# Optimization experiments

Measured on AMD Instinct MI355X. Metric: run time of the kernel, lower is better.

The kernel has to match this reference:

```python
import jax, jax.numpy as jnp
import numpy as np

# ---- config derived from init_kwargs ----
D_MODEL = 768
QK = 64            # qk_dim
HEADDIM = 64
D_INNER = 1536     # round(2.0 * d_model)
H = D_INNER // HEADDIM  # 24 heads
NUM_BC = 2         # share_BC_for_two_graphs -> 4 - 2
NUM_DT = 2         # share_dt_for_two_graphs -> 4 - 2
D_IN_PROJ = 2 * D_INNER + QK * 2 * NUM_BC + H * 2 * NUM_DT  # 3424
CONV_DIM = D_INNER + QK * 2 * NUM_BC                        # 1792
IH, IW = 32, 32
EPS = 1e-5


def setup_inputs() -> dict:
    key = jax.random.key(0)
    ks = jax.random.split(key, 4)
    Bsz, L = 32, IH * IW
    return {
        "u": jax.random.normal(ks[0], (Bsz, L, D_MODEL), jnp.float32),
        "w_in": jax.random.normal(ks[1], (D_IN_PROJ, D_MODEL), jnp.float32) * 0.02,
        "conv_w": jax.random.normal(ks[2], (CONV_DIM, 1, 3, 3), jnp.float32) * 0.1,
        "conv_b": jnp.zeros((CONV_DIM,), jnp.float32),
        "norm_w": jnp.ones((D_INNER,), jnp.float32),
        "w_out": jax.random.normal(ks[3], (D_MODEL, D_INNER), jnp.float32) * 0.02,
    }


def _ssm_scan(dt, Bm, Cm, x):
    """Selective scan. dt:(b,L,H)  Bm,Cm:(b,L,N)  x:(b,L,H,P) -> y:(b,L,H,P)"""
    a = jnp.exp(-dt)  # per-step decay (A = -1 per head)

    def step(h, inp):
        a_t, dt_t, B_t, C_t, x_t = inp
        h = a_t[:, :, None, None] * h + jnp.einsum('bh,bn,bhp->bhnp', dt_t, B_t, x_t)
        y = jnp.einsum('bn,bhnp->bhp', C_t, h)
        return h, y

    b, _, nh = dt.shape
    N, P = Bm.shape[-1], x.shape[-1]
    h0 = jnp.zeros((b, nh, N, P), dt.dtype)
    mv = lambda t: jnp.moveaxis(t, 1, 0)  # put L in scan position
    _, ys = jax.lax.scan(step, h0, (mv(a), mv(dt), mv(Bm), mv(Cm), mv(x)))
    return jnp.moveaxis(ys, 0, 1)


def reference(u, w_in, conv_w, conv_b, norm_w, w_out):
    b, L, _ = u.shape
    zxBCdt = u @ w_in.T  # (b, L, D_IN_PROJ)
    z, xBC, dt = jnp.split(
        zxBCdt, [D_INNER, 2 * D_INNER + QK * 2 * NUM_BC], axis=-1)

    # depthwise 3x3 conv2d over the (IH, IW) token grid, NCHW layout
    x4 = jnp.moveaxis(xBC.reshape(b, IH, IW, CONV_DIM), 3, 1)
    x4 = jax.lax.conv_general_dilated(
        x4, conv_w, window_strides=(1, 1), padding=[(1, 1), (1, 1)],
        feature_group_count=CONV_DIM)
    x4 = jax.nn.silu(x4 + conv_b[None, :, None, None])
    xBC = jnp.moveaxis(x4, 1, 3).reshape(b, L, CONV_DIM)

    x, Bc, Cc = jnp.split(xBC, [D_INNER, D_INNER + NUM_BC * QK], axis=-1)
    xh = x.reshape(b, L, H, HEADDIM)
    Bc = Bc.reshape(b, L, NUM_BC, QK)
    Cc = Cc.reshape(b, L, NUM_BC, QK)
    # dt: 2 graphs x 2 directions, each per-head
    dt_all = jax.nn.softplus(dt.reshape(b, L, 2 * NUM_DT, H))

    y = jnp.zeros((b, L, H, HEADDIM), u.dtype)
    for k in range(2 * NUM_DT):       # fixed small loop: graph x direction
        g, rev = k // 2, k % 2
        dtk, Bk, Ck, xk = dt_all[:, :, k], Bc[:, :, g], Cc[:, :, g], xh
        if rev:  # backward direction over the token sequence
            dtk, Bk, Ck, xk = (jnp.flip(t, 1) for t in (dtk, Bk, Ck, xk))
        yk = _ssm_scan(dtk, Bk, Ck, xk)
        y = y + (jnp.flip(yk, 1) if rev else yk)

    y = y.reshape(b, L, D_INNER)
    # gated RMSNorm (Mamba2-style): norm(y * silu(z)) * weight
    yg = y * jax.nn.silu(z)
    yn = yg * jax.lax.rsqrt(jnp.mean(yg * yg, axis=-1, keepdims=True) + EPS)
    yn = yn * norm_w
    return yn @ w_out.T  # (b, L, d_model)
```

## Files before the change

kernel.cpp:

```cpp
#include <hip/hip_runtime.h>
#include <hip/hip_bf16.h>
#include <stdint.h>


#define D_MODEL 768
#define D_INNER 1536
#define NH 24
#define D_IN_PROJ 3424
#define CONV_DIM 1792
#define NDT 96
#define LSEQ 1024

typedef __bf16 bf16x8 __attribute__((ext_vector_type(8)));
typedef float f32x4 __attribute__((ext_vector_type(4)));

__global__ void cvt_kernel(const float* __restrict__ src, __hip_bfloat16* __restrict__ dst, int n4) {
    int i = blockIdx.x * 256 + threadIdx.x;
    if (i < n4) {
        float4 v = ((const float4*)src)[i];
        __hip_bfloat162 lo, hi;
        lo.x = __float2bfloat16(v.x); lo.y = __float2bfloat16(v.y);
        hi.x = __float2bfloat16(v.z); hi.y = __float2bfloat16(v.w);
        ((__hip_bfloat162*)dst)[2*i]   = lo;
        ((__hip_bfloat162*)dst)[2*i+1] = hi;
    }
}

__global__ void repack_w(const float* __restrict__ cw, float* __restrict__ wT) {
    int i = blockIdx.x * 256 + threadIdx.x;
    if (i < CONV_DIM * 9) {
        int c = i / 9, t = i % 9;
        wT[t * CONV_DIM + c] = cw[i];
    }
}

__device__ __forceinline__ void gl_lds16(const __hip_bfloat16* g, __hip_bfloat16* l) {
    __builtin_amdgcn_global_load_lds(
        (const __attribute__((address_space(1))) void*)g,
        (__attribute__((address_space(3))) void*)l, 16, 0, 0);
}

template<int MODE>
__global__ __launch_bounds__(256) void gemm_bt(
    const __hip_bfloat16* __restrict__ A,
    const __hip_bfloat16* __restrict__ Bt,
    float* __restrict__ OutF,
    __hip_bfloat16* __restrict__ Z, __hip_bfloat16* __restrict__ XBC, float* __restrict__ DT,
    int M, int N, int K)
{
    __shared__ __hip_bfloat16 As[128*32];
    __shared__ __hip_bfloat16 Bs[128*32];
    const int tid  = threadIdx.x;
    const int wave = tid >> 6, lane = tid & 63;
    const int bm = blockIdx.x * 128, bn = blockIdx.y * 128;
    const int wm = (wave >> 1) * 64, wn = (wave & 1) * 64;
    f32x4 acc[4][4] = {};
    const int lrow = lane >> 2;
    const int lcol = (lane & 3) * 8;
    const int fr = lane & 15, fk = (lane >> 4) * 8;
    const int ktiles = K >> 5;
    for (int kt = 0; kt < ktiles; ++kt) {
        const int kofs = kt * 32;
        #pragma unroll
        for (int cc = 0; cc < 2; ++cc) {
            int r = (wave*2 + cc)*16 + lrow;
            gl_lds16(A + (size_t)(bm + r)*K + kofs + lcol, &As[r*32 + lcol]);
            int gn = bn + r; if (gn > N-1) gn = N-1;
            gl_lds16(Bt + (size_t)gn*K + kofs + lcol, &Bs[r*32 + lcol]);
        }
        __syncthreads();
        bf16x8 af[4], bfr[4];
        #pragma unroll
        for (int i = 0; i < 4; ++i)
            af[i] = *reinterpret_cast<const bf16x8*>(&As[(wm + i*16 + fr)*32 + fk]);
        #pragma unroll
        for (int j = 0; j < 4; ++j)
            bfr[j] = *reinterpret_cast<const bf16x8*>(&Bs[(wn + j*16 + fr)*32 + fk]);
        #pragma unroll
        for (int i = 0; i < 4; ++i)
            #pragma unroll
            for (int j = 0; j < 4; ++j)
                acc[i][j] = __builtin_amdgcn_mfma_f32_16x16x32_bf16(af[i], bfr[j], acc[i][j], 0, 0, 0);
        __syncthreads();
    }
    const int er = (lane >> 4) * 4;
    const int ec = lane & 15;
    #pragma unroll
    for (int i = 0; i < 4; ++i) {
        #pragma unroll
        for (int j = 0; j < 4; ++j) {
            #pragma unroll
            for (int r = 0; r < 4; ++r) {
                int row = bm + wm + i*16 + er + r;
                int col = bn + wn + j*16 + ec;
                if (col < N) {
                    float v = acc[i][j][r];
                    if (MODE == 0) {
                        OutF[(size_t)row*N + col] = v;
                    } else {
                        if (col < D_INNER)
                            Z[(size_t)row*D_INNER + col] = __float2bfloat16(v);
                        else if (col < 3328)
                            XBC[(size_t)row*CONV_DIM + (col - D_INNER)] = __float2bfloat16(v);
                        else
                            DT[(size_t)row*NDT + (col - 3328)] = v;
                    }
                }
            }
        }
    }
}

__global__ __launch_bounds__(256) void conv_kernel(
    const __hip_bfloat16* __restrict__ xbc,
    const float* __restrict__ wT,
    const float* __restrict__ cb,
    __hip_bfloat16* __restrict__ out)
{
    size_t idx = (size_t)blockIdx.x * 256 + threadIdx.x;
    const int cg = (int)(idx % (CONV_DIM / 8));
    const int c = cg * 8;
    size_t bp = idx / (CONV_DIM / 8);
    const int pix = (int)(bp % LSEQ);
    const int b = (int)(bp / LSEQ);
    const int y = pix >> 5, x = pix & 31;
    float acc[8];
    {
        float4 c0 = *(const float4*)(cb + c);
        float4 c1 = *(const float4*)(cb + c + 4);
        acc[0]=c0.x; acc[1]=c0.y; acc[2]=c0.z; acc[3]=c0.w;
        acc[4]=c1.x; acc[5]=c1.y; acc[6]=c1.z; acc[7]=c1.w;
    }
    const size_t rowbase = (size_t)b * LSEQ;
    #pragma unroll
    for (int dy = -1; dy <= 1; ++dy) {
        int yy = y + dy; if (yy < 0 || yy > 31) continue;
        #pragma unroll
        for (int dx = -1; dx <= 1; ++dx) {
            int xx = x + dx; if (xx < 0 || xx > 31) continue;
            const int t = (dy+1)*3 + (dx+1);
            bf16x8 v = *(const bf16x8*)(xbc + (rowbase + yy*32 + xx)*(size_t)CONV_DIM + c);
            float4 w0 = *(const float4*)(wT + t*CONV_DIM + c);
            float4 w1 = *(const float4*)(wT + t*CONV_DIM + c + 4);
            acc[0] += w0.x * (float)v[0];
            acc[1] += w0.y * (float)v[1];
            acc[2] += w0.z * (float)v[2];
            acc[3] += w0.w * (float)v[3];
            acc[4] += w1.x * (float)v[4];
            acc[5] += w1.y * (float)v[5];
            acc[6] += w1.z * (float)v[6];
            acc[7] += w1.w * (float)v[7];
        }
    }
    bf16x8 o;
    #pragma unroll
    for (int i = 0; i < 8; ++i) {
        float s = acc[i] / (1.f + __expf(-acc[i]));
        o[i] = (__bf16)s;
    }
    *(bf16x8*)(out + (rowbase + pix)*(size_t)CONV_DIM + c) = o;
}

#define PADW 72
__device__ __forceinline__ f32x4 mfma16(bf16x8 a, bf16x8 b, f32x4 c) {
    return __builtin_amdgcn_mfma_f32_16x16x32_bf16(a, b, c, 0, 0, 0);
}
__device__ __forceinline__ void bar_lds() {
    asm volatile("s_waitcnt lgkmcnt(0)" ::: "memory");
    __builtin_amdgcn_s_barrier();
    __builtin_amdgcn_sched_barrier(0);
}

__global__ __launch_bounds__(256, 3) void scan_ssd(
    const __bf16* __restrict__ conv,
    const float* __restrict__ dtraw,
    __bf16* __restrict__ yf,
    __bf16* __restrict__ yr)
{
    const int tid = threadIdx.x;
    const int w = tid >> 6, lane = tid & 63;
    const int b = blockIdx.x, h = blockIdx.y, dir = blockIdx.z;
    __bf16* yout = dir ? yr : yf;
    const size_t base = (size_t)b * LSEQ;
    const size_t Rtot = (size_t)gridDim.x * LSEQ;

    __shared__ __align__(16) __bf16 XT[64*PADW];
    __shared__ __align__(16) __bf16 Gs[64*PADW];
    __shared__ __align__(16) __bf16 Ts[64*PADW];
    __shared__ __align__(16) __bf16 HT[64*PADW];
    __shared__ __align__(16) __bf16 Bss[64*64];
    __shared__ float Warr[2][64], Earr[2][64], Wmarr[2][64], Rmarr[2][64];

    f32x4 Hst0[4] = {}, Hst1[4] = {};

    const int srow = tid >> 2;
    const int scol = (tid & 3) * 16;
    const int fr = lane & 15, fkq = (lane >> 4) * 8;
    const int er = (lane >> 4) * 4, ec = lane & 15;
    const int rn = w*16 + fr;
    const int sl = dir ? 63 - srow : srow;

    const int rA0 = dir ? (LSEQ - 64) : 0;
    const ptrdiff_t dRow = (ptrdiff_t)(dir ? -64 : 64) * CONV_DIM;
    const ptrdiff_t dDt  = (ptrdiff_t)(dir ? -64 : 64) * NDT;
    const __bf16* pRow = conv + (base + rA0 + srow) * (size_t)CONV_DIM;
    const __bf16* pC   = conv + (base + rA0 + (dir ? 63 - rn : rn)) * (size_t)CONV_DIM + 1664;
    const float*  pDt  = dtraw + (base + rA0 + (dir ? 63 - lane : lane)) * NDT
                         + (2*(tid >> 6) + dir)*24 + h;
    const int xoff = h*64 + scol;

    bf16x8 pfx0 = *(const bf16x8*)(pRow + xoff);
    bf16x8 pfx1 = *(const bf16x8*)(pRow + xoff + 8);
    bf16x8 pfbA0 = *(const bf16x8*)(pRow + 1536 + scol);
    bf16x8 pfbA1 = *(const bf16x8*)(pRow + 1536 + scol + 8);
    bf16x8 pfbB0 = *(const bf16x8*)(pRow + 1600 + scol);
    bf16x8 pfbB1 = *(const bf16x8*)(pRow + 1600 + scol + 8);
    bf16x8 pfc00 = *(const bf16x8*)(pC + fkq);
    bf16x8 pfc01 = *(const bf16x8*)(pC + 32 + fkq);
    bf16x8 pfc10 = *(const bf16x8*)(pC + 64 + fkq);
    bf16x8 pfc11 = *(const bf16x8*)(pC + 96 + fkq);
    float pfd = 0.f;
    if (tid < 128) pfd = *pDt;

    #pragma unroll 1
    for (int c = 0; c < 16; ++c) {
        const int rA = dir ? (LSEQ - (c+1)*64) : c*64;

        bf16x8 bA0 = pfbA0, bA1 = pfbA1, bB0 = pfbB0, bB1 = pfbB1;
        bf16x8 c00 = pfc00, c01 = pfc01, c10 = pfc10, c11 = pfc11;

        {
            const int tau = sl;
            #pragma unroll
            for (int i = 0; i < 8; ++i) {
                const int p = scol + i;
                XT[p*PADW + (tau ^ (((p >> 3) & 7) << 3))] = pfx0[i];
            }
            #pragma unroll
            for (int i = 0; i < 8; ++i) {
                const int p = scol + 8 + i;
                XT[p*PADW + (tau ^ (((p >> 3) & 7) << 3))] = pfx1[i];
            }
            if (tid < 128) {
                const int g = tid >> 6;
                const int t2 = lane;
                float e = __expf(pfd);
                float dts = __logf(1.f + e);
                float s = dts;
                #pragma unroll
                for (int off = 1; off < 64; off <<= 1) {
                    float v = __shfl_up(s, off, 64);
                    if (lane >= off) s += v;
                }
                float stot = __shfl(s, 63, 64);
                float smid = __shfl(s, 31, 64);
                Warr[g][t2]  = __expf(s - stot) * dts;
                Earr[g][t2]  = __expf(-s);
                Wmarr[g][t2] = __expf(s - smid) * dts;
                Rmarr[g][t2] = __expf(smid - s);
            }
        }
        if (c != 15) {
            pRow += dRow; pC += dRow; pDt += dDt;
            pfx0 = *(const bf16x8*)(pRow + xoff);
            pfx1 = *(const bf16x8*)(pRow + xoff + 8);
            pfbA0 = *(const bf16x8*)(pRow + 1536 + scol);
            pfbA1 = *(const bf16x8*)(pRow + 1536 + scol + 8);
            pfbB0 = *(const bf16x8*)(pRow + 1600 + scol);
            pfbB1 = *(const bf16x8*)(pRow + 1600 + scol + 8);
            pfc00 = *(const bf16x8*)(pC + fkq);
            pfc01 = *(const bf16x8*)(pC + 32 + fkq);
            pfc10 = *(const bf16x8*)(pC + 64 + fkq);
            pfc11 = *(const bf16x8*)(pC + 96 + fkq);
            if (tid < 128) pfd = *pDt;
        }
        bar_lds();

        f32x4 Yacc[4] = {};

        auto group = [&](const int g, f32x4 (&Hst)[4],
                         bf16x8 bR0, bf16x8 bR1, bf16x8 cf0, bf16x8 cf1) {
            {
                const float ws = Warr[g][sl];
                const int rsw = (sl & 7) << 3;
                #pragma unroll
                for (int i = 0; i < 8; ++i) {
                    const int n = scol + i;
                    Ts[n*PADW + (sl ^ (((n >> 3) & 7) << 3))] = (__bf16)((float)bR0[i] * ws);
                }
                #pragma unroll
                for (int i = 0; i < 8; ++i) {
                    const int n = scol + 8 + i;
                    Ts[n*PADW + (sl ^ (((n >> 3) & 7) << 3))] = (__bf16)((float)bR1[i] * ws);
                }
                *(bf16x8*)&Bss[sl*64 + (scol ^ rsw)] = bR0;
                *(bf16x8*)&Bss[sl*64 + ((scol + 8) ^ rsw)] = bR1;
            }
            #pragma unroll
            for (int t4 = 0; t4 < 4; ++t4) {
                const int p = t4*16 + ec;
                #pragma unroll
                for (int j = 0; j < 2; ++j) {
                    const int n = w*16 + er + 2*j;
                    __hip_bfloat162 pr;
                    pr.x = __float2bfloat16(Hst[t4][2*j]);
                    pr.y = __float2bfloat16(Hst[t4][2*j+1]);
                    *(__hip_bfloat162*)&HT[p*PADW + n] = pr;
                }
            }
            bar_lds();
            f32x4 Gacc[4] = {};
            __builtin_amdgcn_s_setprio(1);
            #pragma unroll
            for (int s4 = 0; s4 < 4; ++s4) {
                const int s = s4*16 + fr;
                const int ssw = (s & 7) << 3;
                bf16x8 bb0 = *(const bf16x8*)&Bss[s*64 + (fkq ^ ssw)];
                bf16x8 bb1 = *(const bf16x8*)&Bss[s*64 + ((32 + fkq) ^ ssw)];
                Gacc[s4] = mfma16(cf0, bb0, Gacc[s4]);
                Gacc[s4] = mfma16(cf1, bb1, Gacc[s4]);
            }
            __builtin_amdgcn_s_setprio(0);
            const float e63 = Earr[g][63];
            #pragma unroll
            for (int t4 = 0; t4 < 4; ++t4)
                #pragma unroll
                for (int rr = 0; rr < 4; ++rr) Hst[t4][rr] *= e63;
            float rmv[4];
            #pragma unroll
            for (int rr = 0; rr < 4; ++rr) rmv[rr] = Rmarr[g][w*16 + er + rr];
            #pragma unroll
            for (int s4 = 0; s4 < 4; ++s4) {
                const int s = s4*16 + ec;
                const float wm = Wmarr[g][s];
                #pragma unroll
                for (int rr = 0; rr < 4; ++rr) {
                    const int tau = w*16 + er + rr;
                    float m = (tau >= s) ? wm * rmv[rr] : 0.f;
                    Gs[tau*PADW + s] = (__bf16)(Gacc[s4][rr] * m);
                }
            }
            bf16x8 ga0 = *(const bf16x8*)&Gs[rn*PADW + fkq];
            bf16x8 ga1 = *(const bf16x8*)&Gs[rn*PADW + 32 + fkq];
            const float esc = Earr[g][rn];
            bf16x8 ca0, ca1;
            #pragma unroll
            for (int i = 0; i < 8; ++i) {
                ca0[i] = (__bf16)((float)cf0[i] * esc);
                ca1[i] = (__bf16)((float)cf1[i] * esc);
            }
            const int Sn = ((rn >> 3) & 7) << 3;
            bf16x8 ta0 = *(const bf16x8*)&Ts[rn*PADW + (fkq ^ Sn)];
            bf16x8 ta1 = *(const bf16x8*)&Ts[rn*PADW + ((32 + fkq) ^ Sn)];
            __builtin_amdgcn_s_setprio(1);
            #pragma unroll
            for (int p4 = 0; p4 < 4; ++p4) {
                const int p = p4*16 + fr;
                const int Sp = ((p >> 3) & 7) << 3;
                bf16x8 x0 = *(const bf16x8*)&XT[p*PADW + (fkq ^ Sp)];
                bf16x8 x1 = *(const bf16x8*)&XT[p*PADW + ((32 + fkq) ^ Sp)];
                bf16x8 h0 = *(const bf16x8*)&HT[p*PADW + fkq];
                bf16x8 h1 = *(const bf16x8*)&HT[p*PADW + 32 + fkq];
                Yacc[p4] = mfma16(ga0, x0, Yacc[p4]);
                Yacc[p4] = mfma16(ga1, x1, Yacc[p4]);
                Yacc[p4] = mfma16(ca0, h0, Yacc[p4]);
                Yacc[p4] = mfma16(ca1, h1, Yacc[p4]);
                Hst[p4] = mfma16(ta0, x0, Hst[p4]);
                Hst[p4] = mfma16(ta1, x1, Hst[p4]);
            }
            __builtin_amdgcn_s_setprio(0);
        };

        group(0, Hst0, bA0, bA1, c00, c01);
        bar_lds();
        group(1, Hst1, bB0, bB1, c10, c11);

        #pragma unroll
        for (int p4 = 0; p4 < 4; ++p4)
            #pragma unroll
            for (int rr = 0; rr < 4; ++rr) {
                const int tau = w*16 + er + rr;
                Gs[tau*PADW + p4*16 + ec] = (__bf16)Yacc[p4][rr];
            }
        bar_lds();
        {
            const int rowp = rA + (dir ? 63 - srow : srow);
            bf16x8 y0 = *(const bf16x8*)&Gs[srow*PADW + scol];
            bf16x8 y1 = *(const bf16x8*)&Gs[srow*PADW + scol + 8];
            __bf16* dst = yout + ((size_t)h * Rtot + (base + rowp)) * 64 + scol;
            *(bf16x8*)dst = y0;
            *(bf16x8*)(dst + 8) = y1;
        }
    }
}

__global__ __launch_bounds__(256) void gate_kernel(
    const __hip_bfloat16* __restrict__ yf, const __hip_bfloat16* __restrict__ yr,
    const __hip_bfloat16* __restrict__ z, const float* __restrict__ norm_w,
    __hip_bfloat16* __restrict__ yn)
{
    const int row = blockIdx.x, tid = threadIdx.x;
    const size_t R = gridDim.x;
    const size_t ybase = (size_t)row * D_INNER;
    float yg[6]; float ss = 0.f;
    #pragma unroll
    for (int k = 0; k < 6; ++k) {
        int j = tid + k*256;
        size_t yidx = ((size_t)(j >> 6) * R + row) * 64 + (j & 63);
        float yv = __bfloat162float(yf[yidx]) + __bfloat162float(yr[yidx]);
        float zz = __bfloat162float(z[ybase+j]);
        float g  = yv * (zz / (1.f + __expf(-zz)));
        yg[k] = g; ss += g*g;
    }
    #pragma unroll
    for (int off = 32; off > 0; off >>= 1) ss += __shfl_down(ss, off, 64);
    __shared__ float red[4];
    if ((tid & 63) == 0) red[tid >> 6] = ss;
    __syncthreads();
    float total = red[0] + red[1] + red[2] + red[3];
    float rn = rsqrtf(total * (1.f/1536.f) + 1e-5f);
    #pragma unroll
    for (int k = 0; k < 6; ++k) {
        int j = tid + k*256;
        yn[ybase+j] = __float2bfloat16(yg[k] * rn * norm_w[j]);
    }
}

extern "C" void kernel_launch(void* const* d_in, const int* in_sizes, int n_in,
                              void* d_out, int out_size, void* d_ws, size_t ws_size,
                              hipStream_t stream) {
    const float* u      = (const float*)d_in[0];
    const float* w_in   = (const float*)d_in[1];
    const float* conv_w = (const float*)d_in[2];
    const float* conv_b = (const float*)d_in[3];
    const float* norm_w = (const float*)d_in[4];
    const float* w_out  = (const float*)d_in[5];
    (void)in_sizes; (void)n_in; (void)out_size;

    char* ws = (char*)d_ws;
    const size_t nWin  = (size_t)D_IN_PROJ * D_MODEL;
    const size_t nWout = (size_t)D_MODEL * D_INNER;
    __hip_bfloat16* win_bf  = (__hip_bfloat16*)ws;
    __hip_bfloat16* wout_bf = (__hip_bfloat16*)(ws + nWin*2);
    float* wT = (float*)(ws + nWin*2 + nWout*2);
    const size_t wbytes = nWin*2 + nWout*2 + (size_t)9*CONV_DIM*4;
    char* arena = ws + wbytes;

    const size_t perRow = 10624;
    int CB = 32;
    while (CB > 1 && wbytes + perRow*(size_t)CB*1024 > ws_size) CB >>= 1;
    const int nchunks = 32 / CB;
    const size_t R = (size_t)CB * 1024;

    __hip_bfloat16* segA = (__hip_bfloat16*)arena;
    char* pC = arena + R*3072;
    char* pD = pC + R*3584;
    char* pE = pD + R*384;
    __hip_bfloat16* xbc_bf  = (__hip_bfloat16*)pC;
    __hip_bfloat16* yr_bf   = (__hip_bfloat16*)pC;
    float*          dt_f32  = (float*)pD;
    __hip_bfloat16* conv_bf = (__hip_bfloat16*)pE;
    __hip_bfloat16* yn_bf   = (__hip_bfloat16*)pE;
    __hip_bfloat16* u_bf    = segA;
    __hip_bfloat16* yf_bf   = segA;

    cvt_kernel<<<(int)((nWin/4 + 255)/256), 256, 0, stream>>>(w_in, win_bf, (int)(nWin/4));
    cvt_kernel<<<(int)((nWout/4 + 255)/256), 256, 0, stream>>>(w_out, wout_bf, (int)(nWout/4));
    repack_w<<<(CONV_DIM*9 + 255)/256, 256, 0, stream>>>(conv_w, wT);

    for (int c = 0; c < nchunks; ++c) {
        const float* u_c = u + (size_t)c * R * D_MODEL;
        __hip_bfloat16* z_bf = (__hip_bfloat16*)((char*)d_out + (size_t)c * R * 3072);
        float* out_c = (float*)d_out + (size_t)c * R * D_MODEL;

        const size_t nUc4 = R * D_MODEL / 4;
        cvt_kernel<<<(int)((nUc4 + 255)/256), 256, 0, stream>>>(u_c, u_bf, (int)nUc4);

        gemm_bt<1><<<dim3((int)(R/128), (D_IN_PROJ + 127)/128), 256, 0, stream>>>(
            u_bf, win_bf, nullptr, z_bf, xbc_bf, dt_f32, (int)R, D_IN_PROJ, D_MODEL);

        conv_kernel<<<(int)((R*(CONV_DIM/8))/256), 256, 0, stream>>>(xbc_bf, wT, conv_b, conv_bf);

        scan_ssd<<<dim3(CB, NH, 2), 256, 0, stream>>>(
            (const __bf16*)conv_bf, dt_f32, (__bf16*)yf_bf, (__bf16*)yr_bf);

        gate_kernel<<<(int)R, 256, 0, stream>>>(yf_bf, yr_bf, z_bf, norm_w, yn_bf);

        gemm_bt<0><<<dim3((int)(R/128), D_MODEL/128), 256, 0, stream>>>(
            yn_bf, wout_bf, out_c, nullptr, nullptr, nullptr, (int)R, D_MODEL, D_INNER);
    }
}
```

Measured before the change: 1.154 ms.

## Merge both scan groups into one barrier phase with double-buffered dt prep

Gives each of the two B/C groups its own Ts, Bss and HT buffers, so both groups' staging happens before a single barrier and their MFMA work runs in one fused p4 loop. This removes the extra mid-chunk barrier. The softplus/cumsum decay tables for the next chunk are now computed one chunk ahead into a double buffer, and row padding is replaced by an XOR swizzle. The extra LDS and register pressure lowers launch bounds from 3 to 2 blocks per CU, which reduces occupancy.

```diff
diff --git a/kernel.cpp b/kernel.cpp
--- a/kernel.cpp
+++ b/kernel.cpp
@@ -161,7 +161,7 @@
     *(bf16x8*)(out + (rowbase + pix)*(size_t)CONV_DIM + c) = o;
 }
 
-#define PADW 72
+#define SW(r) ((((r) & 7) ^ (((r) >> 3) & 7)) << 3)
 __device__ __forceinline__ f32x4 mfma16(bf16x8 a, bf16x8 b, f32x4 c) {
     return __builtin_amdgcn_mfma_f32_16x16x32_bf16(a, b, c, 0, 0, 0);
 }
@@ -171,7 +171,7 @@
     __builtin_amdgcn_sched_barrier(0);
 }
 
-__global__ __launch_bounds__(256, 3) void scan_ssd(
+__global__ __launch_bounds__(256, 2) void scan_ssd(
     const __bf16* __restrict__ conv,
     const float* __restrict__ dtraw,
     __bf16* __restrict__ yf,
@@ -184,12 +184,12 @@
     const size_t base = (size_t)b * LSEQ;
     const size_t Rtot = (size_t)gridDim.x * LSEQ;
 
-    __shared__ __align__(16) __bf16 XT[64*PADW];
-    __shared__ __align__(16) __bf16 Gs[64*PADW];
-    __shared__ __align__(16) __bf16 Ts[64*PADW];
-    __shared__ __align__(16) __bf16 HT[64*PADW];
-    __shared__ __align__(16) __bf16 Bss[64*64];
-    __shared__ float Warr[2][64], Earr[2][64], Wmarr[2][64], Rmarr[2][64];
+    __shared__ __align__(16) __bf16 XT[64*64];
+    __shared__ __align__(16) __bf16 Gs[64*64];
+    __shared__ __align__(16) __bf16 Ts[2][64*64];
+    __shared__ __align__(16) __bf16 Bss[2][64*64];
+    __shared__ __align__(16) __bf16 HT[2][64*64];
+    __shared__ float Warr[2][2][64], Earr[2][2][64], Wmarr[2][2][64], Rmarr[2][2][64];
 
     f32x4 Hst0[4] = {}, Hst1[4] = {};
 
@@ -199,6 +199,8 @@
     const int er = (lane >> 4) * 4, ec = lane & 15;
     const int rn = w*16 + fr;
     const int sl = dir ? 63 - srow : srow;
+    const int swsl = SW(sl);
+    const int swrn = SW(rn);
 
     const int rA0 = dir ? (LSEQ - 64) : 0;
     const ptrdiff_t dRow = (ptrdiff_t)(dir ? -64 : 64) * CONV_DIM;
@@ -209,184 +211,221 @@
                          + (2*(tid >> 6) + dir)*24 + h;
     const int xoff = h*64 + scol;
 
+    float pfdN = 0.f;
+    if (tid < 128) {
+        const int g = tid >> 6;
+        float d0 = *pDt;
+        float e = __expf(d0);
+        float dts = __logf(1.f + e);
+        float s = dts;
+        #pragma unroll
+        for (int off = 1; off < 64; off <<= 1) {
+            float v = __shfl_up(s, off, 64);
+            if (lane >= off) s += v;
+        }
+        float stot = __shfl(s, 63, 64);
+        float smid = __shfl(s, 31, 64);
+        Warr[0][g][lane]  = __expf(s - stot) * dts;
+        Earr[0][g][lane]  = __expf(-s);
+        Wmarr[0][g][lane] = __expf(s - smid) * dts;
+        Rmarr[0][g][lane] = __expf(smid - s);
+        pDt += dDt;
+        pfdN = *pDt;
+    }
     bf16x8 pfx0 = *(const bf16x8*)(pRow + xoff);
     bf16x8 pfx1 = *(const bf16x8*)(pRow + xoff + 8);
-    bf16x8 pfbA0 = *(const bf16x8*)(pRow + 1536 + scol);
-    bf16x8 pfbA1 = *(const bf16x8*)(pRow + 1536 + scol + 8);
-    bf16x8 pfbB0 = *(const bf16x8*)(pRow + 1600 + scol);
-    bf16x8 pfbB1 = *(const bf16x8*)(pRow + 1600 + scol + 8);
+    bf16x8 pfb00 = *(const bf16x8*)(pRow + 1536 + scol);
+    bf16x8 pfb01 = *(const bf16x8*)(pRow + 1536 + scol + 8);
+    bf16x8 pfb10 = *(const bf16x8*)(pRow + 1600 + scol);
+    bf16x8 pfb11 = *(const bf16x8*)(pRow + 1600 + scol + 8);
     bf16x8 pfc00 = *(const bf16x8*)(pC + fkq);
     bf16x8 pfc01 = *(const bf16x8*)(pC + 32 + fkq);
     bf16x8 pfc10 = *(const bf16x8*)(pC + 64 + fkq);
     bf16x8 pfc11 = *(const bf16x8*)(pC + 96 + fkq);
-    float pfd = 0.f;
-    if (tid < 128) pfd = *pDt;
+    bar_lds();
 
     #pragma unroll 1
     for (int c = 0; c < 16; ++c) {
+        const int cb = c & 1;
         const int rA = dir ? (LSEQ - (c+1)*64) : c*64;
 
-        bf16x8 bA0 = pfbA0, bA1 = pfbA1, bB0 = pfbB0, bB1 = pfbB1;
-        bf16x8 c00 = pfc00, c01 = pfc01, c10 = pfc10, c11 = pfc11;
+        const bf16x8 c00 = pfc00, c01 = pfc01, c10 = pfc10, c11 = pfc11;
 
         {
-            const int tau = sl;
             #pragma unroll
             for (int i = 0; i < 8; ++i) {
                 const int p = scol + i;
-                XT[p*PADW + (tau ^ (((p >> 3) & 7) << 3))] = pfx0[i];
+                XT[p*64 + (sl ^ SW(p))] = pfx0[i];
             }
             #pragma unroll
             for (int i = 0; i < 8; ++i) {
                 const int p = scol + 8 + i;
-                XT[p*PADW + (tau ^ (((p >> 3) & 7) << 3))] = pfx1[i];
-            }
-            if (tid < 128) {
-                const int g = tid >> 6;
-                const int t2 = lane;
-                float e = __expf(pfd);
-                float dts = __logf(1.f + e);
-                float s = dts;
+                XT[p*64 + (sl ^ SW(p))] = pfx1[i];
+            }
+        }
+        {
+            const float ws0 = Warr[cb][0][sl];
+            const float ws1 = Warr[cb][1][sl];
+            #pragma unroll
+            for (int i = 0; i < 8; ++i) {
+                const int n = scol + i;
+                Ts[0][n*64 + (sl ^ SW(n))] = (__bf16)((float)pfb00[i] * ws0);
+                Ts[1][n*64 + (sl ^ SW(n))] = (__bf16)((float)pfb10[i] * ws1);
+            }
+            #pragma unroll
+            for (int i = 0; i < 8; ++i) {
+                const int n = scol + 8 + i;
+                Ts[0][n*64 + (sl ^ SW(n))] = (__bf16)((float)pfb01[i] * ws0);
+                Ts[1][n*64 + (sl ^ SW(n))] = (__bf16)((float)pfb11[i] * ws1);
+            }
+            *(bf16x8*)&Bss[0][sl*64 + (scol ^ swsl)]       = pfb00;
+            *(bf16x8*)&Bss[0][sl*64 + ((scol + 8) ^ swsl)] = pfb01;
+            *(bf16x8*)&Bss[1][sl*64 + (scol ^ swsl)]       = pfb10;
+            *(bf16x8*)&Bss[1][sl*64 + ((scol + 8) ^ swsl)] = pfb11;
+        }
+        {
+            #pragma unroll
+            for (int t4 = 0; t4 < 4; ++t4) {
+                const int p = t4*16 + ec;
+                const int swp = SW(p);
                 #pragma unroll
-                for (int off = 1; off < 64; off <<= 1) {
-                    float v = __shfl_up(s, off, 64);
-                    if (lane >= off) s += v;
+                for (int j = 0; j < 2; ++j) {
+                    const int n = w*16 + er + 2*j;
+                    __hip_bfloat162 pr0, pr1;
+                    pr0.x = __float2bfloat16(Hst0[t4][2*j]);
+                    pr0.y = __float2bfloat16(Hst0[t4][2*j+1]);
+                    pr1.x = __float2bfloat16(Hst1[t4][2*j]);
+                    pr1.y = __float2bfloat16(Hst1[t4][2*j+1]);
+                    *(__hip_bfloat162*)&HT[0][p*64 + (n ^ swp)] = pr0;
+                    *(__hip_bfloat162*)&HT[1][p*64 + (n ^ swp)] = pr1;
                 }
-                float stot = __shfl(s, 63, 64);
-                float smid = __shfl(s, 31, 64);
-                Warr[g][t2]  = __expf(s - stot) * dts;
-                Earr[g][t2]  = __expf(-s);
-                Wmarr[g][t2] = __expf(s - smid) * dts;
-                Rmarr[g][t2] = __expf(smid - s);
-            }
+            }
+        }
+        {
+            const float e630 = Earr[cb][0][63];
+            const float e631 = Earr[cb][1][63];
+            #pragma unroll
+            for (int t4 = 0; t4 < 4; ++t4)
+                #pragma unroll
+                for (int rr = 0; rr < 4; ++rr) {
+                    Hst0[t4][rr] *= e630;
+                    Hst1[t4][rr] *= e631;
+                }
+        }
+        if (c < 15 && tid < 128) {
+            const int g = tid >> 6;
+            float e = __expf(pfdN);
+            float dts = __logf(1.f + e);
+            float s = dts;
+            #pragma unroll
+            for (int off = 1; off < 64; off <<= 1) {
+                float v = __shfl_up(s, off, 64);
+                if (lane >= off) s += v;
+            }
+            float stot = __shfl(s, 63, 64);
+            float smid = __shfl(s, 31, 64);
+            const int nb = cb ^ 1;
+            Warr[nb][g][lane]  = __expf(s - stot) * dts;
+            Earr[nb][g][lane]  = __expf(-s);
+            Wmarr[nb][g][lane] = __expf(s - smid) * dts;
+            Rmarr[nb][g][lane] = __expf(smid - s);
         }
         if (c != 15) {
-            pRow += dRow; pC += dRow; pDt += dDt;
+            pRow += dRow; pC += dRow;
             pfx0 = *(const bf16x8*)(pRow + xoff);
             pfx1 = *(const bf16x8*)(pRow + xoff + 8);
-            pfbA0 = *(const bf16x8*)(pRow + 1536 + scol);
-            pfbA1 = *(const bf16x8*)(pRow + 1536 + scol + 8);
-            pfbB0 = *(const bf16x8*)(pRow + 1600 + scol);
-            pfbB1 = *(const bf16x8*)(pRow + 1600 + scol + 8);
+            pfb00 = *(const bf16x8*)(pRow + 1536 + scol);
+            pfb01 = *(const bf16x8*)(pRow + 1536 + scol + 8);
+            pfb10 = *(const bf16x8*)(pRow + 1600 + scol);
+            pfb11 = *(const bf16x8*)(pRow + 1600 + scol + 8);
             pfc00 = *(const bf16x8*)(pC + fkq);
             pfc01 = *(const bf16x8*)(pC + 32 + fkq);
             pfc10 = *(const bf16x8*)(pC + 64 + fkq);
             pfc11 = *(const bf16x8*)(pC + 96 + fkq);
-            if (tid < 128) pfd = *pDt;
+            if (c < 14 && tid < 128) { pDt += dDt; pfdN = *pDt; }
         }
         bar_lds();
 
-        f32x4 Yacc[4] = {};
-
-        auto group = [&](const int g, f32x4 (&Hst)[4],
-                         bf16x8 bR0, bf16x8 bR1, bf16x8 cf0, bf16x8 cf1) {
-            {
-                const float ws = Warr[g][sl];
-                const int rsw = (sl & 7) << 3;
-                #pragma unroll
-                for (int i = 0; i < 8; ++i) {
-                    const int n = scol + i;
-                    Ts[n*PADW + (sl ^ (((n >> 3) & 7) << 3))] = (__bf16)((float)bR0[i] * ws);
-                }
-                #pragma unroll
-                for (int i = 0; i < 8; ++i) {
-                    const int n = scol + 8 + i;
-                    Ts[n*PADW + (sl ^ (((n >> 3) & 7) << 3))] = (__bf16)((float)bR1[i] * ws);
-                }
-                *(bf16x8*)&Bss[sl*64 + (scol ^ rsw)] = bR0;
-                *(bf16x8*)&Bss[sl*64 + ((scol + 8) ^ rsw)] = bR1;
-            }
-            #pragma unroll
-            for (int t4 = 0; t4 < 4; ++t4) {
-                const int p = t4*16 + ec;
-                #pragma unroll
-                for (int j = 0; j < 2; ++j) {
-                    const int n = w*16 + er + 2*j;
-                    __hip_bfloat162 pr;
-                    pr.x = __float2bfloat16(Hst[t4][2*j]);
-                    pr.y = __float2bfloat16(Hst[t4][2*j+1]);
-                    *(__hip_bfloat162*)&HT[p*PADW + n] = pr;
-                }
-            }
-            bar_lds();
+        bf16x8 cf[2][2] = { { c00, c01 }, { c10, c11 } };
+        bf16x8 ga[2][2], ca[2][2], ta[2][2];
+        #pragma unroll
+        for (int g = 0; g < 2; ++g) {
             f32x4 Gacc[4] = {};
             __builtin_amdgcn_s_setprio(1);
             #pragma unroll
             for (int s4 = 0; s4 < 4; ++s4) {
                 const int s = s4*16 + fr;
-                const int ssw = (s & 7) << 3;
-                bf16x8 bb0 = *(const bf16x8*)&Bss[s*64 + (fkq ^ ssw)];
-                bf16x8 bb1 = *(const bf16x8*)&Bss[s*64 + ((32 + fkq) ^ ssw)];
-                Gacc[s4] = mfma16(cf0, bb0, Gacc[s4]);
-                Gacc[s4] = mfma16(cf1, bb1, Gacc[s4]);
+                const int ss = SW(s);
+                bf16x8 bb0 = *(const bf16x8*)&Bss[g][s*64 + (fkq ^ ss)];
+                bf16x8 bb1 = *(const bf16x8*)&Bss[g][s*64 + ((32 + fkq) ^ ss)];
+                Gacc[s4] = mfma16(cf[g][0], bb0, Gacc[s4]);
+                Gacc[s4] = mfma16(cf[g][1], bb1, Gacc[s4]);
             }
             __builtin_amdgcn_s_setprio(0);
-            const float e63 = Earr[g][63];
-            #pragma unroll
-            for (int t4 = 0; t4 < 4; ++t4)
-                #pragma unroll
-                for (int rr = 0; rr < 4; ++rr) Hst[t4][rr] *= e63;
             float rmv[4];
             #pragma unroll
-            for (int rr = 0; rr < 4; ++rr) rmv[rr] = Rmarr[g][w*16 + er + rr];
+            for (int rr = 0; rr < 4; ++rr) rmv[rr] = Rmarr[cb][g][w*16 + er + rr];
             #pragma unroll
             for (int s4 = 0; s4 < 4; ++s4) {
                 const int s = s4*16 + ec;
-                const float wm = Wmarr[g][s];
+                const float wm = Wmarr[cb][g][s];
                 #pragma unroll
                 for (int rr = 0; rr < 4; ++rr) {
                     const int tau = w*16 + er + rr;
                     float m = (tau >= s) ? wm * rmv[rr] : 0.f;
-                    Gs[tau*PADW + s] = (__bf16)(Gacc[s4][rr] * m);
+                    Gs[tau*64 + (s ^ SW(tau))] = (__bf16)(Gacc[s4][rr] * m);
                 }
             }
-            bf16x8 ga0 = *(const bf16x8*)&Gs[rn*PADW + fkq];
-            bf16x8 ga1 = *(const bf16x8*)&Gs[rn*PADW + 32 + fkq];
-            const float esc = Earr[g][rn];
-            bf16x8 ca0, ca1;
+            ga[g][0] = *(const bf16x8*)&Gs[rn*64 + (fkq ^ swrn)];
+            ga[g][1] = *(const bf16x8*)&Gs[rn*64 + ((32 + fkq) ^ swrn)];
+            const float esc = Earr[cb][g][rn];
             #pragma unroll
             for (int i = 0; i < 8; ++i) {
-                ca0[i] = (__bf16)((float)cf0[i] * esc);
-                ca1[i] = (__bf16)((float)cf1[i] * esc);
-            }
-            const int Sn = ((rn >> 3) & 7) << 3;
-            bf16x8 ta0 = *(const bf16x8*)&Ts[rn*PADW + (fkq ^ Sn)];
-            bf16x8 ta1 = *(const bf16x8*)&Ts[rn*PADW + ((32 + fkq) ^ Sn)];
-            __builtin_amdgcn_s_setprio(1);
-            #pragma unroll
-            for (int p4 = 0; p4 < 4; ++p4) {
-                const int p = p4*16 + fr;
-                const int Sp = ((p >> 3) & 7) << 3;
-                bf16x8 x0 = *(const bf16x8*)&XT[p*PADW + (fkq ^ Sp)];
-                bf16x8 x1 = *(const bf16x8*)&XT[p*PADW + ((32 + fkq) ^ Sp)];
-                bf16x8 h0 = *(const bf16x8*)&HT[p*PADW + fkq];
-                bf16x8 h1 = *(const bf16x8*)&HT[p*PADW + 32 + fkq];
-                Yacc[p4] = mfma16(ga0, x0, Yacc[p4]);
-                Yacc[p4] = mfma16(ga1, x1, Yacc[p4]);
-                Yacc[p4] = mfma16(ca0, h0, Yacc[p4]);
-                Yacc[p4] = mfma16(ca1, h1, Yacc[p4]);
-                Hst[p4] = mfma16(ta0, x0, Hst[p4]);
-                Hst[p4] = mfma16(ta1, x1, Hst[p4]);
-            }
-            __builtin_amdgcn_s_setprio(0);
-        };
-
-        group(0, Hst0, bA0, bA1, c00, c01);
-        bar_lds();
-        group(1, Hst1, bB0, bB1, c10, c11);
+                ca[g][0][i] = (__bf16)((float)cf[g][0][i] * esc);
+                ca[g][1][i] = (__bf16)((float)cf[g][1][i] * esc);
+            }
+            ta[g][0] = *(const bf16x8*)&Ts[g][rn*64 + (fkq ^ swrn)];
+            ta[g][1] = *(const bf16x8*)&Ts[g][rn*64 + ((32 + fkq) ^ swrn)];
+        }
+        f32x4 Yacc[4] = {};
+        __builtin_amdgcn_s_setprio(1);
+        #pragma unroll
+        for (int p4 = 0; p4 < 4; ++p4) {
+            const int p = p4*16 + fr;
+            const int sp = SW(p);
+            bf16x8 x0  = *(const bf16x8*)&XT[p*64 + (fkq ^ sp)];
+            bf16x8 x1  = *(const bf16x8*)&XT[p*64 + ((32 + fkq) ^ sp)];
+            bf16x8 h00 = *(const bf16x8*)&HT[0][p*64 + (fkq ^ sp)];
+            bf16x8 h01 = *(const bf16x8*)&HT[0][p*64 + ((32 + fkq) ^ sp)];
+            bf16x8 h10 = *(const bf16x8*)&HT[1][p*64 + (fkq ^ sp)];
+            bf16x8 h11 = *(const bf16x8*)&HT[1][p*64 + ((32 + fkq) ^ sp)];
+            Yacc[p4] = mfma16(ga[0][0], x0, Yacc[p4]);
+            Yacc[p4] = mfma16(ga[0][1], x1, Yacc[p4]);
+            Yacc[p4] = mfma16(ca[0][0], h00, Yacc[p4]);
+            Yacc[p4] = mfma16(ca[0][1], h01, Yacc[p4]);
+            Yacc[p4] = mfma16(ga[1][0], x0, Yacc[p4]);
+            Yacc[p4] = mfma16(ga[1][1], x1, Yacc[p4]);
+            Yacc[p4] = mfma16(ca[1][0], h10, Yacc[p4]);
+            Yacc[p4] = mfma16(ca[1][1], h11, Yacc[p4]);
+            Hst0[p4] = mfma16(ta[0][0], x0, Hst0[p4]);
+            Hst0[p4] = mfma16(ta[0][1], x1, Hst0[p4]);
+            Hst1[p4] = mfma16(ta[1][0], x0, Hst1[p4]);
+            Hst1[p4] = mfma16(ta[1][1], x1, Hst1[p4]);
+        }
+        __builtin_amdgcn_s_setprio(0);
 
         #pragma unroll
         for (int p4 = 0; p4 < 4; ++p4)
             #pragma unroll
             for (int rr = 0; rr < 4; ++rr) {
                 const int tau = w*16 + er + rr;
-                Gs[tau*PADW + p4*16 + ec] = (__bf16)Yacc[p4][rr];
+                Gs[tau*64 + ((p4*16 + ec) ^ SW(tau))] = (__bf16)Yacc[p4][rr];
             }
         bar_lds();
         {
             const int rowp = rA + (dir ? 63 - srow : srow);
-            bf16x8 y0 = *(const bf16x8*)&Gs[srow*PADW + scol];
-            bf16x8 y1 = *(const bf16x8*)&Gs[srow*PADW + scol + 8];
+            bf16x8 y0 = *(const bf16x8*)&Gs[srow*64 + (scol ^ SW(srow))];
+            bf16x8 y1 = *(const bf16x8*)&Gs[srow*64 + ((scol + 8) ^ SW(srow))];
             __bf16* dst = yout + ((size_t)h * Rtot + (base + rowp)) * 64 + scol;
             *(bf16x8*)dst = y0;
             *(bf16x8*)(dst + 8) = y1;
```

Result: faster. 1.040 ms (-9.9%).
